# Kernel optimization log

Hardware: AMD Instinct MI355X
Metric: run time of the kernel (lower is better)

Reference implementation:

```python
import jax, jax.numpy as jnp
import numpy as np

DIM = 512
CHUNK = 64
LN_EPS = 1e-5


def setup_inputs() -> dict:
    key = jax.random.key(0)
    ks = jax.random.split(key, 9)
    B, S, D = 4, 4096, DIM
    x = jax.random.normal(ks[0], (B, S, D), dtype=jnp.float32)
    # Linear weights stored as [in, out] (equivalent to torch W.T)
    W_omega = jax.random.normal(ks[1], (D, D), dtype=jnp.float32) / np.sqrt(D)
    b_omega = jnp.zeros((D,), dtype=jnp.float32)
    log_scale = jnp.full((D,), np.log(0.1), dtype=jnp.float32)
    ln_gamma = jnp.ones((4 * D,), dtype=jnp.float32)
    ln_beta = jnp.zeros((4 * D,), dtype=jnp.float32)
    W1 = jax.random.normal(ks[2], (4 * D, 2 * D), dtype=jnp.float32) / np.sqrt(4 * D)
    b1 = jnp.zeros((2 * D,), dtype=jnp.float32)
    W2 = jax.random.normal(ks[3], (2 * D, D), dtype=jnp.float32) / np.sqrt(2 * D)
    b2 = jnp.zeros((D,), dtype=jnp.float32)
    return {"x": x, "W_omega": W_omega, "b_omega": b_omega, "log_scale": log_scale,
            "ln_gamma": ln_gamma, "ln_beta": ln_beta, "W1": W1, "b1": b1, "W2": W2, "b2": b2}


def reference(x, W_omega, b_omega, log_scale, ln_gamma, ln_beta, W1, b1, W2, b2):
    B, S, D = x.shape
    C = CHUNK
    # S chosen as multiple of C, so pad_len == 0 (matches torch no-pad branch)
    N = S // C
    omega = x @ W_omega + b_omega                      # [B,S,D]
    oc = omega.reshape(B, N, C, D)
    xc = x.reshape(B, N, C, D)
    pos = jnp.arange(1, C + 1, dtype=x.dtype)          # [C]
    pos_scale = (1.0 / jnp.sqrt(pos))[None, None, :, None]
    scale = jnp.exp(log_scale)
    phi = jnp.cumsum(oc * scale * pos_scale, axis=2)   # [B,N,C,D]
    cos_phi = jnp.cos(phi)
    sin_phi = jnp.sin(phi)
    cr = xc * cos_phi                                   # content modulated real
    ci = xc * sin_phi                                   # content modulated imag
    pos_norm = pos[None, None, :, None]
    mr = jnp.cumsum(cr, axis=2) / pos_norm              # memory real
    mi = jnp.cumsum(ci, axis=2) / pos_norm              # memory imag
    rr = mr * cos_phi + mi * sin_phi                    # retrieved real
    ri = mi * cos_phi - mr * sin_phi                    # retrieved imag
    ctx = jnp.concatenate([cr.reshape(B, S, D), ci.reshape(B, S, D),
                           rr.reshape(B, S, D), ri.reshape(B, S, D)], axis=-1)  # [B,S,4D]
    mu = jnp.mean(ctx, axis=-1, keepdims=True)
    var = jnp.mean((ctx - mu) ** 2, axis=-1, keepdims=True)
    h = (ctx - mu) / jnp.sqrt(var + LN_EPS) * ln_gamma + ln_beta
    h = h @ W1 + b1
    h = jax.nn.gelu(h, approximate=False)               # torch GELU default = exact erf
    out = h @ W2 + b2                                   # dropout is identity at eval
    return x + out
```

## Files before the change

kernel.cpp:

```cpp
#include <hip/hip_runtime.h>
#include <hip/hip_bf16.h>
#include <math.h>


typedef __bf16 bf16x8 __attribute__((ext_vector_type(8)));
typedef __bf16 bf16x4 __attribute__((ext_vector_type(4)));
typedef __bf16 bf16x2 __attribute__((ext_vector_type(2)));
typedef float  f32x4  __attribute__((ext_vector_type(4)));

typedef __attribute__((address_space(1))) void* gas_ptr;
typedef __attribute__((address_space(3))) void* las_ptr;

__device__ __forceinline__ void load_lds16(const void* g, void* l) {
    __builtin_amdgcn_global_load_lds((gas_ptr)g, (las_ptr)l, 16, 0, 0);
}

__device__ __forceinline__ void transpose_tile(const float* __restrict__ in,
                                               __bf16* __restrict__ out,
                                               int K, int N, int bx, int by,
                                               float (*tile)[33])
{
    const int tid = threadIdx.x;
    const int tx = tid & 31, ty = tid >> 5;
    const int n0 = bx * 32, k0 = by * 32;
    #pragma unroll
    for (int i = 0; i < 32; i += 8)
        tile[ty + i][tx] = in[(size_t)(k0 + ty + i) * N + n0 + tx];
    __syncthreads();
    #pragma unroll
    for (int i = 0; i < 32; i += 8)
        out[(size_t)(n0 + ty + i) * K + k0 + tx] = (__bf16)tile[tx][ty + i];
}

__global__ __launch_bounds__(256)
void prep_kernel(const float* __restrict__ x, __bf16* __restrict__ xb,
                 const float* __restrict__ W_omega, __bf16* __restrict__ womT,
                 const float* __restrict__ W1, __bf16* __restrict__ w1T,
                 const float* __restrict__ W2, __bf16* __restrict__ w2T)
{
    __shared__ float tile[32][33];
    const int bid = blockIdx.x;
    if (bid < 8192) {
        int i = bid * 256 + threadIdx.x;
        float4 v = ((const float4*)x)[i];
        bf16x4 o = { (__bf16)v.x, (__bf16)v.y, (__bf16)v.z, (__bf16)v.w };
        ((bf16x4*)xb)[i] = o;
    } else if (bid < 8448) {
        int t = bid - 8192;
        transpose_tile(W_omega, womT, 512, 512, t & 15, t >> 4, tile);
    } else if (bid < 10496) {
        int t = bid - 8448;
        transpose_tile(W1, w1T, 2048, 1024, t & 31, t >> 5, tile);
    } else {
        int t = bid - 10496;
        transpose_tile(W2, w2T, 1024, 512, t & 15, t >> 4, tile);
    }
}

template<int MODE>
__global__ __launch_bounds__(256)
void gemm_kernel(const __bf16* __restrict__ A, const __bf16* __restrict__ Bt,
                 const float* __restrict__ bias, const __bf16* __restrict__ resid,
                 void* __restrict__ out, int M, int N, int K)
{
    __shared__ __bf16 As[2][128 * 64];
    __shared__ __bf16 Bs[2][128 * 64];

    const int tid     = threadIdx.x;
    const int tiles_n = N >> 7;
    const int ln_tn   = __ffs(tiles_n) - 1;
    const int per_m   = (M >> 7) >> 3;

    const int xcd = blockIdx.x & 7;
    const int j   = blockIdx.x >> 3;
    const int tile_m = (xcd * per_m + (j >> ln_tn)) << 7;
    const int tile_n = (j & (tiles_n - 1)) << 7;

    const int wave = tid >> 6;
    const int lane = tid & 63;

    const int srow = lane >> 3;
    const int scol = ((lane & 7) ^ srow) << 3;

    const __bf16* Ags = A  + (size_t)(tile_m + wave * 32 + srow) * K + scol;
    const __bf16* Bgs = Bt + (size_t)(tile_n + wave * 32 + srow) * K + scol;

    const int m0 = (wave >> 1) << 6;
    const int n0 = (wave & 1) << 6;
    const int lr = lane & 15;
    const int q  = lane >> 4;
    const int l7 = lane & 7;
    const int fc0 = ((0 + q) ^ l7) << 3;
    const int fc1 = ((4 + q) ^ l7) << 3;

    f32x4 acc[4][4];
    #pragma unroll
    for (int i = 0; i < 4; ++i)
        #pragma unroll
        for (int jj = 0; jj < 4; ++jj)
            acc[i][jj] = (f32x4){0.f, 0.f, 0.f, 0.f};

    const int nIter = K >> 6;

    #pragma unroll
    for (int c = 0; c < 4; ++c) {
        load_lds16(Ags + (size_t)(c * 8) * K, &As[0][(wave * 32 + c * 8) * 64]);
        load_lds16(Bgs + (size_t)(c * 8) * K, &Bs[0][(wave * 32 + c * 8) * 64]);
    }

    for (int it = 0; it < nIter; ++it) {
        const int cur = it & 1;
        __syncthreads();
        if (it + 1 < nIter) {
            const int nk = (it + 1) << 6;
            #pragma unroll
            for (int c = 0; c < 4; ++c) {
                load_lds16(Ags + nk + (size_t)(c * 8) * K, &As[cur ^ 1][(wave * 32 + c * 8) * 64]);
                load_lds16(Bgs + nk + (size_t)(c * 8) * K, &Bs[cur ^ 1][(wave * 32 + c * 8) * 64]);
            }
        }

        const __bf16* as = As[cur];
        const __bf16* bs = Bs[cur];
        {
            bf16x8 af[4], bq[4];
            #pragma unroll
            for (int i = 0; i < 4; ++i)
                af[i] = *(const bf16x8*)&as[(m0 + i * 16 + lr) * 64 + fc0];
            #pragma unroll
            for (int jj = 0; jj < 4; ++jj)
                bq[jj] = *(const bf16x8*)&bs[(n0 + jj * 16 + lr) * 64 + fc0];
            #pragma unroll
            for (int i = 0; i < 4; ++i)
                #pragma unroll
                for (int jj = 0; jj < 4; ++jj)
                    acc[i][jj] = __builtin_amdgcn_mfma_f32_16x16x32_bf16(af[i], bq[jj], acc[i][jj], 0, 0, 0);
        }
        {
            bf16x8 af[4], bq[4];
            #pragma unroll
            for (int i = 0; i < 4; ++i)
                af[i] = *(const bf16x8*)&as[(m0 + i * 16 + lr) * 64 + fc1];
            #pragma unroll
            for (int jj = 0; jj < 4; ++jj)
                bq[jj] = *(const bf16x8*)&bs[(n0 + jj * 16 + lr) * 64 + fc1];
            #pragma unroll
            for (int i = 0; i < 4; ++i)
                #pragma unroll
                for (int jj = 0; jj < 4; ++jj)
                    acc[i][jj] = __builtin_amdgcn_mfma_f32_16x16x32_bf16(af[i], bq[jj], acc[i][jj], 0, 0, 0);
        }
    }

    const int orow0 = tile_m + m0 + (q << 2);
    const int ocol0 = tile_n + n0 + lr;
    #pragma unroll
    for (int i = 0; i < 4; ++i) {
        #pragma unroll
        for (int jj = 0; jj < 4; ++jj) {
            const int col = ocol0 + jj * 16;
            const float bv = bias[col];
            #pragma unroll
            for (int r = 0; r < 4; ++r) {
                const int row = orow0 + i * 16 + r;
                float v = acc[i][jj][r] + bv;
                size_t idx = (size_t)row * N + col;
                if (MODE == 0) {
                    ((__bf16*)out)[idx] = (__bf16)v;
                } else if (MODE == 1) {
                    float g = 0.5f * v * (1.0f + erff(v * 0.70710678118654752f));
                    ((__bf16*)out)[idx] = (__bf16)g;
                } else {
                    ((float*)out)[idx] = v + (float)resid[idx];
                }
            }
        }
    }
}

template<int MODE>
__global__ __launch_bounds__(512, 1)
void gemm256_kernel(const __bf16* __restrict__ A, const __bf16* __restrict__ Bt,
                    const float* __restrict__ bias, void* __restrict__ out,
                    int M, int N, int K)
{
    __shared__ __bf16 As[4][256 * 32];
    __shared__ __bf16 Bs[4][256 * 32];

    const int tid  = threadIdx.x;
    const int wv   = tid >> 6;
    const int lane = tid & 63;
    const int wm   = wv >> 2;
    const int wn   = wv & 3;

    const int tiles_n = N >> 8;
    const int ln_tn   = __ffs(tiles_n) - 1;
    const int per_m   = (M >> 8) >> 3;

    const int xcd = blockIdx.x & 7;
    const int j   = blockIdx.x >> 3;
    const int tile_m = (xcd * per_m + (j >> ln_tn)) << 8;
    const int tile_n = (j & (tiles_n - 1)) << 8;

    const int srow = 16 * wv + (lane >> 2);
    const int sig8 = (((lane & 3) ^ ((lane >> 3) & 3)) << 3);

    const __bf16* Ag = A  + (size_t)(tile_m + srow) * K + sig8;
    const __bf16* Bg = Bt + (size_t)(tile_n + srow) * K + sig8;
    const size_t rowK128 = (size_t)128 * K;
    const int lbase = wv * 512;

    const int lr    = lane & 15;
    const int q4    = lane >> 4;
    const int fslot = ((q4 ^ ((lane >> 1) & 3)) << 3);
    const int arow0 = wm * 128 + lr;
    const int brow0 = wn * 64 + lr;

    const unsigned ldsA0 = (unsigned)(size_t)(las_ptr)&As[0][0];
    const unsigned ldsB0 = (unsigned)(size_t)(las_ptr)&Bs[0][0];
    const unsigned asA = ldsA0 + (unsigned)((arow0 * 32 + fslot) << 1);
    const unsigned asB = ldsB0 + (unsigned)((brow0 * 32 + fslot) << 1);

    f32x4 acc[8][4];
    #pragma unroll
    for (int i = 0; i < 8; ++i)
        #pragma unroll
        for (int jj = 0; jj < 4; ++jj)
            acc[i][jj] = (f32x4){0.f, 0.f, 0.f, 0.f};

    const int NKS = K >> 5;

    auto stage = [&](int ks) {
        const int slot = ks & 3;
        const __bf16* ag = Ag + (ks << 5);
        const __bf16* bg = Bg + (ks << 5);
        load_lds16(ag,           &As[slot][lbase]);
        load_lds16(ag + rowK128, &As[slot][4096 + lbase]);
        load_lds16(bg,           &Bs[slot][lbase]);
        load_lds16(bg + rowK128, &Bs[slot][4096 + lbase]);
    };

    bf16x8 afA[8], bqA[4], afB[8], bqB[4];

#define DSR(d, a, o) asm volatile("ds_read_b128 %0, %1 offset:" o \
                                  : "=v"(d) : "v"(a))
#define SB __builtin_amdgcn_sched_barrier(0)
#define MM4(CAF, CBQ, I)                                                      \
    acc[I][0] = __builtin_amdgcn_mfma_f32_16x16x32_bf16(CAF[I], CBQ[0], acc[I][0], 0, 0, 0); \
    acc[I][1] = __builtin_amdgcn_mfma_f32_16x16x32_bf16(CAF[I], CBQ[1], acc[I][1], 0, 0, 0); \
    acc[I][2] = __builtin_amdgcn_mfma_f32_16x16x32_bf16(CAF[I], CBQ[2], acc[I][2], 0, 0, 0); \
    acc[I][3] = __builtin_amdgcn_mfma_f32_16x16x32_bf16(CAF[I], CBQ[3], acc[I][3], 0, 0, 0);

#define G256_READ(KS, NAF, NBQ)                                               \
    {                                                                         \
        const unsigned aA_ = asA + (unsigned)(((KS) & 3) << 14);              \
        const unsigned aB_ = asB + (unsigned)(((KS) & 3) << 14);              \
        DSR(NAF[0], aA_, "0");    DSR(NAF[1], aA_, "1024");                   \
        DSR(NAF[2], aA_, "2048"); DSR(NAF[3], aA_, "3072");                   \
        DSR(NAF[4], aA_, "4096"); DSR(NAF[5], aA_, "5120");                   \
        DSR(NAF[6], aA_, "6144"); DSR(NAF[7], aA_, "7168");                   \
        DSR(NBQ[0], aB_, "0");    DSR(NBQ[1], aB_, "1024");                   \
        DSR(NBQ[2], aB_, "2048"); DSR(NBQ[3], aB_, "3072");                   \
    }

#define G256_PHASE_FULL(KS, CAF, CBQ, NAF, NBQ)                               \
    {                                                                         \
        const int ks_ = (KS);                                                 \
        asm volatile("s_waitcnt vmcnt(8)" ::: "memory");                      \
        __builtin_amdgcn_s_barrier();                                         \
        asm volatile("" ::: "memory");                                        \
        const int slot_ = (ks_ + 4) & 3;                                      \
        const __bf16* ag_ = Ag + ((ks_ + 4) << 5);                            \
        const __bf16* bg_ = Bg + ((ks_ + 4) << 5);                            \
        const unsigned aA_ = asA + (unsigned)(((ks_ + 1) & 3) << 14);         \
        const unsigned aB_ = asB + (unsigned)(((ks_ + 1) & 3) << 14);         \
        __builtin_amdgcn_s_setprio(1);                                        \
        load_lds16(ag_,           &As[slot_][lbase]);                         \
        MM4(CAF, CBQ, 0) SB;                                                  \
        load_lds16(ag_ + rowK128, &As[slot_][4096 + lbase]);                  \
        MM4(CAF, CBQ, 1) SB;                                                  \
        load_lds16(bg_,           &Bs[slot_][lbase]);                         \
        MM4(CAF, CBQ, 2) SB;                                                  \
        load_lds16(bg_ + rowK128, &Bs[slot_][4096 + lbase]);                  \
        MM4(CAF, CBQ, 3) SB;                                                  \
        DSR(NAF[0], aA_, "0"); DSR(NAF[1], aA_, "1024");                      \
        DSR(NAF[2], aA_, "2048");                                             \
        MM4(CAF, CBQ, 4) SB;                                                  \
        DSR(NAF[3], aA_, "3072"); DSR(NAF[4], aA_, "4096");                   \
        DSR(NAF[5], aA_, "5120");                                             \
        MM4(CAF, CBQ, 5) SB;                                                  \
        DSR(NAF[6], aA_, "6144"); DSR(NAF[7], aA_, "7168");                   \
        DSR(NBQ[0], aB_, "0");                                                \
        MM4(CAF, CBQ, 6) SB;                                                  \
        DSR(NBQ[1], aB_, "1024"); DSR(NBQ[2], aB_, "2048");                   \
        DSR(NBQ[3], aB_, "3072");                                             \
        MM4(CAF, CBQ, 7)                                                      \
        __builtin_amdgcn_s_setprio(0);                                        \
        asm volatile("s_waitcnt lgkmcnt(0)" ::: "memory");                    \
        __builtin_amdgcn_sched_barrier(0);                                    \
    }

#define G256_PHASE_TAIL(KS, CAF, CBQ, NAF, NBQ)                               \
    {                                                                         \
        const int ks_ = (KS);                                                 \
        const int r_  = NKS - 1 - ks_;                                        \
        if (r_ >= 3)      asm volatile("s_waitcnt vmcnt(8)" ::: "memory");    \
        else if (r_ == 2) asm volatile("s_waitcnt vmcnt(4)" ::: "memory");    \
        else if (r_ == 1) asm volatile("s_waitcnt vmcnt(0)" ::: "memory");    \
        __builtin_amdgcn_s_barrier();                                         \
        asm volatile("" ::: "memory");                                        \
        if (ks_ + 4 < NKS) stage(ks_ + 4);                                    \
        if (ks_ + 1 < NKS) G256_READ(ks_ + 1, NAF, NBQ)                       \
        __builtin_amdgcn_s_setprio(1);                                        \
        _Pragma("unroll")                                                     \
        for (int i_ = 0; i_ < 8; ++i_)                                        \
            _Pragma("unroll")                                                 \
            for (int j_ = 0; j_ < 4; ++j_)                                    \
                acc[i_][j_] = __builtin_amdgcn_mfma_f32_16x16x32_bf16(        \
                    CAF[i_], CBQ[j_], acc[i_][j_], 0, 0, 0);                  \
        __builtin_amdgcn_s_setprio(0);                                        \
        asm volatile("s_waitcnt lgkmcnt(0)" ::: "memory");                    \
        __builtin_amdgcn_sched_barrier(0);                                    \
    }

    stage(0); stage(1); stage(2);
    asm volatile("s_waitcnt vmcnt(8)" ::: "memory");
    __builtin_amdgcn_s_barrier();
    asm volatile("" ::: "memory");
    stage(3);
    G256_READ(0, afA, bqA)
    asm volatile("s_waitcnt lgkmcnt(0)" ::: "memory");
    __builtin_amdgcn_sched_barrier(0);

    int ks = 0;
    for (; ks + 6 < NKS; ks += 2) {
        G256_PHASE_FULL(ks,     afA, bqA, afB, bqB)
        G256_PHASE_FULL(ks + 1, afB, bqB, afA, bqA)
    }
    for (; ks < NKS; ks += 2) {
        G256_PHASE_TAIL(ks,     afA, bqA, afB, bqB)
        G256_PHASE_TAIL(ks + 1, afB, bqB, afA, bqA)
    }

#undef G256_PHASE_FULL
#undef G256_PHASE_TAIL
#undef G256_READ
#undef MM4
#undef SB
#undef DSR

    const int orow0 = tile_m + wm * 128 + (q4 << 2);
    const int ocol0 = tile_n + wn * 64 + lr;
    #pragma unroll
    for (int i = 0; i < 8; ++i) {
        #pragma unroll
        for (int jj = 0; jj < 4; ++jj) {
            const int col = ocol0 + jj * 16;
            const float bv = bias[col];
            #pragma unroll
            for (int r = 0; r < 4; ++r) {
                const int row = orow0 + i * 16 + r;
                float v = acc[i][jj][r] + bv;
                if (MODE == 1) {
                    float g = 0.5f * v * (1.0f + erff(v * 0.70710678118654752f));
                    ((__bf16*)out)[(size_t)row * N + col] = (__bf16)g;
                } else {
                    ((__bf16*)out)[(size_t)row * N + col] = (__bf16)v;
                }
            }
        }
    }
}

__global__ __launch_bounds__(256)
void scan_ln_kernel(const __bf16* __restrict__ xb, const __bf16* __restrict__ omega,
                    const float* __restrict__ log_scale,
                    const float* __restrict__ gamma, const float* __restrict__ beta,
                    __bf16* __restrict__ ctx)
{
    const int chunk = blockIdx.x;
    const int tid   = threadIdx.x;
    const int lane  = tid & 63, wv = tid >> 6;
    const int d0    = tid << 1;
    const size_t base = (size_t)chunk * 64 * 512;

    float scale[2], g0[2], g1[2], g2[2], g3[2], e0[2], e1[2], e2[2], e3[2];
    #pragma unroll
    for (int u = 0; u < 2; ++u) {
        const int d = d0 + u;
        scale[u] = expf(log_scale[d]);
        g0[u] = gamma[d]; g1[u] = gamma[512 + d]; g2[u] = gamma[1024 + d]; g3[u] = gamma[1536 + d];
        e0[u] = beta[d];  e1[u] = beta[512 + d];  e2[u] = beta[1024 + d];  e3[u] = beta[1536 + d];
    }

    float phi[2] = {0.f, 0.f}, scr[2] = {0.f, 0.f}, sci[2] = {0.f, 0.f};
    __shared__ float red[2][8];

    bf16x2 om_n = *(const bf16x2*)&omega[base + d0];
    bf16x2 xv_n = *(const bf16x2*)&xb[base + d0];

    for (int c = 0; c < 64; ++c) {
        const bf16x2 omv = om_n;
        const bf16x2 xvv = xv_n;
        if (c < 63) {
            om_n = *(const bf16x2*)&omega[base + (size_t)(c + 1) * 512 + d0];
            xv_n = *(const bf16x2*)&xb[base + (size_t)(c + 1) * 512 + d0];
        }
        const float rsq = rsqrtf((float)(c + 1));
        const float inv = 1.0f / (float)(c + 1);

        float cr[2], ci[2], rr[2], ri[2];
        float s = 0.f, s2 = 0.f;
        #pragma unroll
        for (int u = 0; u < 2; ++u) {
            const float om = (float)omv[u];
            const float xv = (float)xvv[u];
            phi[u] += om * scale[u] * rsq;
            float sp, cp;
            __sincosf(phi[u], &sp, &cp);
            cr[u] = xv * cp; ci[u] = xv * sp;
            scr[u] += cr[u]; sci[u] += ci[u];
            const float mr = scr[u] * inv, mi = sci[u] * inv;
            rr[u] = mr * cp + mi * sp;
            ri[u] = mi * cp - mr * sp;
            s  += cr[u] + ci[u] + rr[u] + ri[u];
            s2 += cr[u]*cr[u] + ci[u]*ci[u] + rr[u]*rr[u] + ri[u]*ri[u];
        }
        #pragma unroll
        for (int o = 32; o > 0; o >>= 1) {
            s  += __shfl_xor(s, o);
            s2 += __shfl_xor(s2, o);
        }
        if (lane == 0) { red[c & 1][wv] = s; red[c & 1][4 + wv] = s2; }
        __syncthreads();
        const float S  = red[c & 1][0] + red[c & 1][1] + red[c & 1][2] + red[c & 1][3];
        const float S2 = red[c & 1][4] + red[c & 1][5] + red[c & 1][6] + red[c & 1][7];
        const float mu   = S * (1.0f / 2048.0f);
        const float var  = S2 * (1.0f / 2048.0f) - mu * mu;
        const float rstd = rsqrtf(var + 1e-5f);

        const size_t ob = ((size_t)chunk * 64 + c) * 2048;
        bf16x2 o0, o1, o2, o3;
        #pragma unroll
        for (int u = 0; u < 2; ++u) {
            o0[u] = (__bf16)(((cr[u] - mu) * rstd) * g0[u] + e0[u]);
            o1[u] = (__bf16)(((ci[u] - mu) * rstd) * g1[u] + e1[u]);
            o2[u] = (__bf16)(((rr[u] - mu) * rstd) * g2[u] + e2[u]);
            o3[u] = (__bf16)(((ri[u] - mu) * rstd) * g3[u] + e3[u]);
        }
        *(bf16x2*)&ctx[ob + d0]        = o0;
        *(bf16x2*)&ctx[ob + 512 + d0]  = o1;
        *(bf16x2*)&ctx[ob + 1024 + d0] = o2;
        *(bf16x2*)&ctx[ob + 1536 + d0] = o3;
    }
}

extern "C" void kernel_launch(void* const* d_in, const int* in_sizes, int n_in,
                              void* d_out, int out_size, void* d_ws, size_t ws_size,
                              hipStream_t stream)
{
    const float* x         = (const float*)d_in[0];
    const float* W_omega   = (const float*)d_in[1];
    const float* b_omega   = (const float*)d_in[2];
    const float* log_scale = (const float*)d_in[3];
    const float* ln_gamma  = (const float*)d_in[4];
    const float* ln_beta   = (const float*)d_in[5];
    const float* W1        = (const float*)d_in[6];
    const float* b1        = (const float*)d_in[7];
    const float* W2        = (const float*)d_in[8];
    const float* b2        = (const float*)d_in[9];
    float* out = (float*)d_out;

    char* ws = (char*)d_ws;
    __bf16* xb    = (__bf16*)(ws);
    __bf16* womT  = (__bf16*)(ws + 16777216);
    __bf16* w1T   = (__bf16*)(ws + 17301504);
    __bf16* w2T   = (__bf16*)(ws + 21495808);
    __bf16* omega = (__bf16*)(ws + 22544384);
    __bf16* hbuf  = (__bf16*)(ws + 22544384);
    __bf16* ctx   = (__bf16*)(ws + 56098816);

    prep_kernel<<<11008, 256, 0, stream>>>(x, xb, W_omega, womT, W1, w1T, W2, w2T);

    gemm_kernel<0><<<512, 256, 0, stream>>>(xb, womT, b_omega, nullptr, omega, 16384, 512, 512);

    scan_ln_kernel<<<256, 256, 0, stream>>>(xb, omega, log_scale, ln_gamma, ln_beta, ctx);

    gemm256_kernel<1><<<256, 512, 0, stream>>>(ctx, w1T, b1, hbuf, 16384, 1024, 2048);

    gemm_kernel<2><<<512, 256, 0, stream>>>(hbuf, w2T, b2, xb, out, 16384, 512, 1024);
}
```

Baseline: 263.8 us.

## Rewrite 128-wide GEMM as 256x128 tile with 4-stage LDS pipeline

Replaces the double-buffered 128x128 GEMM used for the omega projection and the final W2 projection with a 512-thread, 256x128-tile kernel. It uses a 4-deep ring of K=32 LDS stages, a vmcnt-based wait, hand-scheduled ds_read_b128, and interleaved MFMA groups with setprio and sched_barrier. The aim is better latency hiding and fewer barriers per K step, plus a larger M tile to reuse B. Risks: the grid halves to 256 blocks at one block per CU, and hand-coded waitcnt logic makes it fragile.

```diff
diff --git a/kernel.cpp b/kernel.cpp
--- a/kernel.cpp
+++ b/kernel.cpp
@@ -58,40 +58,47 @@
 }
 
 template<int MODE>
-__global__ __launch_bounds__(256)
-void gemm_kernel(const __bf16* __restrict__ A, const __bf16* __restrict__ Bt,
-                 const float* __restrict__ bias, const __bf16* __restrict__ resid,
-                 void* __restrict__ out, int M, int N, int K)
+__global__ __launch_bounds__(512, 1)
+void gemm128_kernel(const __bf16* __restrict__ A, const __bf16* __restrict__ Bt,
+                    const float* __restrict__ bias, const __bf16* __restrict__ resid,
+                    void* __restrict__ out, int M, int N, int K)
 {
-    __shared__ __bf16 As[2][128 * 64];
-    __shared__ __bf16 Bs[2][128 * 64];
-
-    const int tid     = threadIdx.x;
+    __shared__ __bf16 As[4][256 * 32];
+    __shared__ __bf16 Bs[4][128 * 32];
+
+    const int tid  = threadIdx.x;
+    const int wv   = tid >> 6;
+    const int lane = tid & 63;
+    const int wm   = wv >> 1;
+    const int wn   = wv & 1;
+
     const int tiles_n = N >> 7;
     const int ln_tn   = __ffs(tiles_n) - 1;
-    const int per_m   = (M >> 7) >> 3;
+    const int per_m   = (M >> 8) >> 3;
 
     const int xcd = blockIdx.x & 7;
     const int j   = blockIdx.x >> 3;
-    const int tile_m = (xcd * per_m + (j >> ln_tn)) << 7;
+    const int tile_m = (xcd * per_m + (j >> ln_tn)) << 8;
     const int tile_n = (j & (tiles_n - 1)) << 7;
 
-    const int wave = tid >> 6;
-    const int lane = tid & 63;
-
-    const int srow = lane >> 3;
-    const int scol = ((lane & 7) ^ srow) << 3;
-
-    const __bf16* Ags = A  + (size_t)(tile_m + wave * 32 + srow) * K + scol;
-    const __bf16* Bgs = Bt + (size_t)(tile_n + wave * 32 + srow) * K + scol;
-
-    const int m0 = (wave >> 1) << 6;
-    const int n0 = (wave & 1) << 6;
-    const int lr = lane & 15;
-    const int q  = lane >> 4;
-    const int l7 = lane & 7;
-    const int fc0 = ((0 + q) ^ l7) << 3;
-    const int fc1 = ((4 + q) ^ l7) << 3;
+    const int srow = 16 * wv + (lane >> 2);
+    const int sig8 = (((lane & 3) ^ ((lane >> 3) & 3)) << 3);
+
+    const __bf16* Ag = A  + (size_t)(tile_m + srow) * K + sig8;
+    const __bf16* Bg = Bt + (size_t)(tile_n + srow) * K + sig8;
+    const size_t rowK128 = (size_t)128 * K;
+    const int lbase = wv * 512;
+
+    const int lr    = lane & 15;
+    const int q4    = lane >> 4;
+    const int fslot = ((q4 ^ ((lane >> 1) & 3)) << 3);
+    const int arow0 = wm * 64 + lr;
+    const int brow0 = wn * 64 + lr;
+
+    const unsigned ldsA0 = (unsigned)(size_t)(las_ptr)&As[0][0];
+    const unsigned ldsB0 = (unsigned)(size_t)(las_ptr)&Bs[0][0];
+    const unsigned asA = ldsA0 + (unsigned)((arow0 * 32 + fslot) << 1);
+    const unsigned asB = ldsB0 + (unsigned)((brow0 * 32 + fslot) << 1);
 
     f32x4 acc[4][4];
     #pragma unroll
@@ -100,60 +107,117 @@
         for (int jj = 0; jj < 4; ++jj)
             acc[i][jj] = (f32x4){0.f, 0.f, 0.f, 0.f};
 
-    const int nIter = K >> 6;
-
-    #pragma unroll
-    for (int c = 0; c < 4; ++c) {
-        load_lds16(Ags + (size_t)(c * 8) * K, &As[0][(wave * 32 + c * 8) * 64]);
-        load_lds16(Bgs + (size_t)(c * 8) * K, &Bs[0][(wave * 32 + c * 8) * 64]);
-    }
-
-    for (int it = 0; it < nIter; ++it) {
-        const int cur = it & 1;
-        __syncthreads();
-        if (it + 1 < nIter) {
-            const int nk = (it + 1) << 6;
-            #pragma unroll
-            for (int c = 0; c < 4; ++c) {
-                load_lds16(Ags + nk + (size_t)(c * 8) * K, &As[cur ^ 1][(wave * 32 + c * 8) * 64]);
-                load_lds16(Bgs + nk + (size_t)(c * 8) * K, &Bs[cur ^ 1][(wave * 32 + c * 8) * 64]);
-            }
-        }
-
-        const __bf16* as = As[cur];
-        const __bf16* bs = Bs[cur];
-        {
-            bf16x8 af[4], bq[4];
-            #pragma unroll
-            for (int i = 0; i < 4; ++i)
-                af[i] = *(const bf16x8*)&as[(m0 + i * 16 + lr) * 64 + fc0];
-            #pragma unroll
-            for (int jj = 0; jj < 4; ++jj)
-                bq[jj] = *(const bf16x8*)&bs[(n0 + jj * 16 + lr) * 64 + fc0];
-            #pragma unroll
-            for (int i = 0; i < 4; ++i)
-                #pragma unroll
-                for (int jj = 0; jj < 4; ++jj)
-                    acc[i][jj] = __builtin_amdgcn_mfma_f32_16x16x32_bf16(af[i], bq[jj], acc[i][jj], 0, 0, 0);
-        }
-        {
-            bf16x8 af[4], bq[4];
-            #pragma unroll
-            for (int i = 0; i < 4; ++i)
-                af[i] = *(const bf16x8*)&as[(m0 + i * 16 + lr) * 64 + fc1];
-            #pragma unroll
-            for (int jj = 0; jj < 4; ++jj)
-                bq[jj] = *(const bf16x8*)&bs[(n0 + jj * 16 + lr) * 64 + fc1];
-            #pragma unroll
-            for (int i = 0; i < 4; ++i)
-                #pragma unroll
-                for (int jj = 0; jj < 4; ++jj)
-                    acc[i][jj] = __builtin_amdgcn_mfma_f32_16x16x32_bf16(af[i], bq[jj], acc[i][jj], 0, 0, 0);
-        }
-    }
-
-    const int orow0 = tile_m + m0 + (q << 2);
-    const int ocol0 = tile_n + n0 + lr;
+    const int NKS = K >> 5;
+
+    auto stage = [&](int ks) {
+        const int slot = ks & 3;
+        const __bf16* ag = Ag + (ks << 5);
+        const __bf16* bg = Bg + (ks << 5);
+        load_lds16(ag,           &As[slot][lbase]);
+        load_lds16(ag + rowK128, &As[slot][4096 + lbase]);
+        load_lds16(bg,           &Bs[slot][lbase]);
+    };
+
+    bf16x8 afA[4], bqA[4], afB[4], bqB[4];
+
+#define DSR(d, a, o) asm volatile("ds_read_b128 %0, %1 offset:" o \
+                                  : "=v"(d) : "v"(a))
+#define SB __builtin_amdgcn_sched_barrier(0)
+#define MM4(CAF, CBQ, I)                                                      \
+    acc[I][0] = __builtin_amdgcn_mfma_f32_16x16x32_bf16(CAF[I], CBQ[0], acc[I][0], 0, 0, 0); \
+    acc[I][1] = __builtin_amdgcn_mfma_f32_16x16x32_bf16(CAF[I], CBQ[1], acc[I][1], 0, 0, 0); \
+    acc[I][2] = __builtin_amdgcn_mfma_f32_16x16x32_bf16(CAF[I], CBQ[2], acc[I][2], 0, 0, 0); \
+    acc[I][3] = __builtin_amdgcn_mfma_f32_16x16x32_bf16(CAF[I], CBQ[3], acc[I][3], 0, 0, 0);
+
+#define G128_READ(KS, NAF, NBQ)                                               \
+    {                                                                         \
+        const unsigned aA_ = asA + (unsigned)(((KS) & 3) << 14);              \
+        const unsigned aB_ = asB + (unsigned)(((KS) & 3) << 13);              \
+        DSR(NAF[0], aA_, "0");    DSR(NAF[1], aA_, "1024");                   \
+        DSR(NAF[2], aA_, "2048"); DSR(NAF[3], aA_, "3072");                   \
+        DSR(NBQ[0], aB_, "0");    DSR(NBQ[1], aB_, "1024");                   \
+        DSR(NBQ[2], aB_, "2048"); DSR(NBQ[3], aB_, "3072");                   \
+    }
+
+#define G128_PHASE_FULL(KS, CAF, CBQ, NAF, NBQ)                               \
+    {                                                                         \
+        const int ks_ = (KS);                                                 \
+        asm volatile("s_waitcnt vmcnt(6)" ::: "memory");                      \
+        __builtin_amdgcn_s_barrier();                                         \
+        asm volatile("" ::: "memory");                                        \
+        const int slot_ = (ks_ + 4) & 3;                                      \
+        const __bf16* ag_ = Ag + ((ks_ + 4) << 5);                            \
+        const __bf16* bg_ = Bg + ((ks_ + 4) << 5);                            \
+        const unsigned aA_ = asA + (unsigned)(((ks_ + 1) & 3) << 14);         \
+        const unsigned aB_ = asB + (unsigned)(((ks_ + 1) & 3) << 13);         \
+        __builtin_amdgcn_s_setprio(1);                                        \
+        load_lds16(ag_,           &As[slot_][lbase]);                         \
+        MM4(CAF, CBQ, 0) SB;                                                  \
+        load_lds16(ag_ + rowK128, &As[slot_][4096 + lbase]);                  \
+        load_lds16(bg_,           &Bs[slot_][lbase]);                         \
+        MM4(CAF, CBQ, 1) SB;                                                  \
+        DSR(NAF[0], aA_, "0");    DSR(NAF[1], aA_, "1024");                   \
+        DSR(NAF[2], aA_, "2048"); DSR(NAF[3], aA_, "3072");                   \
+        MM4(CAF, CBQ, 2) SB;                                                  \
+        DSR(NBQ[0], aB_, "0");    DSR(NBQ[1], aB_, "1024");                   \
+        DSR(NBQ[2], aB_, "2048"); DSR(NBQ[3], aB_, "3072");                   \
+        MM4(CAF, CBQ, 3)                                                      \
+        __builtin_amdgcn_s_setprio(0);                                        \
+        asm volatile("s_waitcnt lgkmcnt(0)" ::: "memory");                    \
+        __builtin_amdgcn_sched_barrier(0);                                    \
+    }
+
+#define G128_PHASE_TAIL(KS, CAF, CBQ, NAF, NBQ)                               \
+    {                                                                         \
+        const int ks_ = (KS);                                                 \
+        const int r_  = NKS - 1 - ks_;                                        \
+        if (r_ >= 3)      asm volatile("s_waitcnt vmcnt(6)" ::: "memory");    \
+        else if (r_ == 2) asm volatile("s_waitcnt vmcnt(3)" ::: "memory");    \
+        else if (r_ == 1) asm volatile("s_waitcnt vmcnt(0)" ::: "memory");    \
+        __builtin_amdgcn_s_barrier();                                         \
+        asm volatile("" ::: "memory");                                        \
+        if (ks_ + 4 < NKS) stage(ks_ + 4);                                    \
+        if (ks_ + 1 < NKS) G128_READ(ks_ + 1, NAF, NBQ)                       \
+        __builtin_amdgcn_s_setprio(1);                                        \
+        _Pragma("unroll")                                                     \
+        for (int i_ = 0; i_ < 4; ++i_)                                        \
+            _Pragma("unroll")                                                 \
+            for (int j_ = 0; j_ < 4; ++j_)                                    \
+                acc[i_][j_] = __builtin_amdgcn_mfma_f32_16x16x32_bf16(        \
+                    CAF[i_], CBQ[j_], acc[i_][j_], 0, 0, 0);                  \
+        __builtin_amdgcn_s_setprio(0);                                        \
+        asm volatile("s_waitcnt lgkmcnt(0)" ::: "memory");                    \
+        __builtin_amdgcn_sched_barrier(0);                                    \
+    }
+
+    stage(0); stage(1); stage(2);
+    asm volatile("s_waitcnt vmcnt(6)" ::: "memory");
+    __builtin_amdgcn_s_barrier();
+    asm volatile("" ::: "memory");
+    stage(3);
+    G128_READ(0, afA, bqA)
+    asm volatile("s_waitcnt lgkmcnt(0)" ::: "memory");
+    __builtin_amdgcn_sched_barrier(0);
+
+    int ks = 0;
+    for (; ks + 6 < NKS; ks += 2) {
+        G128_PHASE_FULL(ks,     afA, bqA, afB, bqB)
+        G128_PHASE_FULL(ks + 1, afB, bqB, afA, bqA)
+    }
+    for (; ks < NKS; ks += 2) {
+        G128_PHASE_TAIL(ks,     afA, bqA, afB, bqB)
+        G128_PHASE_TAIL(ks + 1, afB, bqB, afA, bqA)
+    }
+
+#undef G128_PHASE_FULL
+#undef G128_PHASE_TAIL
+#undef G128_READ
+#undef MM4
+#undef SB
+#undef DSR
+
+    const int orow0 = tile_m + wm * 64 + (q4 << 2);
+    const int ocol0 = tile_n + wn * 64 + lr;
     #pragma unroll
     for (int i = 0; i < 4; ++i) {
         #pragma unroll
@@ -167,9 +231,6 @@
                 size_t idx = (size_t)row * N + col;
                 if (MODE == 0) {
                     ((__bf16*)out)[idx] = (__bf16)v;
-                } else if (MODE == 1) {
-                    float g = 0.5f * v * (1.0f + erff(v * 0.70710678118654752f));
-                    ((__bf16*)out)[idx] = (__bf16)g;
                 } else {
                     ((float*)out)[idx] = v + (float)resid[idx];
                 }
@@ -482,11 +543,11 @@
 
     prep_kernel<<<11008, 256, 0, stream>>>(x, xb, W_omega, womT, W1, w1T, W2, w2T);
 
-    gemm_kernel<0><<<512, 256, 0, stream>>>(xb, womT, b_omega, nullptr, omega, 16384, 512, 512);
+    gemm128_kernel<0><<<256, 512, 0, stream>>>(xb, womT, b_omega, nullptr, omega, 16384, 512, 512);
 
     scan_ln_kernel<<<256, 256, 0, stream>>>(xb, omega, log_scale, ln_gamma, ln_beta, ctx);
 
     gemm256_kernel<1><<<256, 512, 0, stream>>>(ctx, w1T, b1, hbuf, 16384, 1024, 2048);
 
-    gemm_kernel<2><<<512, 256, 0, stream>>>(hbuf, w2T, b2, xb, out, 16384, 512, 1024);
-}
+    gemm128_kernel<2><<<256, 512, 0, stream>>>(hbuf, w2T, b2, xb, out, 16384, 512, 1024);
+}
```

New measurement: 258.8 us. No clear change (-1.9%).
